# Kernel optimization log

Measured on AMD Instinct MI355X. Metric: run time of the kernel, lower is better.

Reference implementation:

```python
import jax, jax.numpy as jnp
import numpy as np

HIDDEN = 1024
MSG = 1024
T = 3
B = 256
N = 80  # num_categories


def setup_inputs() -> dict:
    key = jax.random.key(0)
    ks = jax.random.split(key, 10)
    s = 0.02
    return {
        "x": jax.random.normal(ks[0], (B, N), dtype=jnp.float32),
        # msg_update_fn: Linear(hidden->msg) + ReLU
        "W1": jax.random.normal(ks[1], (MSG, HIDDEN), dtype=jnp.float32) * s,
        "b1": jax.random.normal(ks[2], (MSG,), dtype=jnp.float32) * s,
        # GRUCell(msg_dim -> hidden_dim), torch layout [3*hidden, in]
        "Wih": jax.random.normal(ks[3], (3 * HIDDEN, MSG), dtype=jnp.float32) * s,
        "Whh": jax.random.normal(ks[4], (3 * HIDDEN, HIDDEN), dtype=jnp.float32) * s,
        "bih": jax.random.normal(ks[5], (3 * HIDDEN,), dtype=jnp.float32) * s,
        "bhh": jax.random.normal(ks[6], (3 * HIDDEN,), dtype=jnp.float32) * s,
        # Conv1d(hidden, 1, kernel=1) == per-position linear projection
        "w_s": jax.random.normal(ks[7], (HIDDEN,), dtype=jnp.float32) * s,
        "b_s": jax.random.normal(ks[8], (), dtype=jnp.float32) * s,
    }


def _gru_cell(msg, h, Wih, Whh, bih, bhh):
    # torch GRUCell: gate order (r, z, n)
    gi = msg @ Wih.T + bih  # [rows, 3H]
    gh = h @ Whh.T + bhh
    i_r, i_z, i_n = jnp.split(gi, 3, axis=-1)
    h_r, h_z, h_n = jnp.split(gh, 3, axis=-1)
    r = jax.nn.sigmoid(i_r + h_r)
    z = jax.nn.sigmoid(i_z + h_z)
    n = jnp.tanh(i_n + r * h_n)
    return (1.0 - z) * n + z * h


def reference(x, W1, b1, Wih, Whh, bih, bhh, w_s, b_s):
    batch, num_cat = x.shape
    pad_left = (HIDDEN - 1) // 2
    # hidden_0: each scalar label embedded at position pad_left of a zero vector
    hidden = jnp.zeros((batch, num_cat, HIDDEN), dtype=x.dtype).at[:, :, pad_left].set(x)
    for _ in range(T):
        m = jax.nn.relu(jnp.einsum("bnh,mh->bnm", hidden, W1) + b1)  # [B,N,MSG]
        # all-pairs masked mean over j != i  ==  (total sum - self) / (N-1)
        msg = (jnp.sum(m, axis=1, keepdims=True) - m) / (num_cat - 1)
        hidden = _gru_cell(
            msg.reshape(-1, MSG), hidden.reshape(-1, HIDDEN), Wih, Whh, bih, bhh
        ).reshape(batch, num_cat, HIDDEN)
    # Conv1d(hidden->1, k=1) over [B, hidden, N] then squeeze -> [B, N]
    return jnp.einsum("bnh,h->bn", hidden, w_s) + b_s
```

## Files before the change

kernel.cpp:

```cpp
#include <hip/hip_runtime.h>
#include <cstdint>
#include <cstddef>

#define HID 1024
#define NB 256
#define NCAT 80
#define ROWS (NB*NCAT)
#define PADL 511

typedef short short8_t __attribute__((ext_vector_type(8)));
typedef float f32x4_t __attribute__((ext_vector_type(4)));
typedef unsigned short u16;
typedef u16 u16x8_t __attribute__((ext_vector_type(8)));
typedef u16 u16x4_t __attribute__((ext_vector_type(4)));
typedef float f32x4v_t __attribute__((ext_vector_type(4)));

typedef const __attribute__((address_space(1))) unsigned int guint_t;
typedef __attribute__((address_space(3))) unsigned int luint_t;

__device__ __forceinline__ void gl_lds16(const void* g, void* l) {
  __builtin_amdgcn_global_load_lds((guint_t*)g, (luint_t*)l, 16, 0, 0);
}

__device__ __forceinline__ u16 f2bf(float f) {
  unsigned u = __float_as_uint(f);
  u += 0x7fffu + ((u >> 16) & 1u);
  return (u16)(u >> 16);
}
__device__ __forceinline__ float bf2f(u16 s) {
  return __uint_as_float(((unsigned)s) << 16);
}

__device__ __forceinline__ f32x4_t mfma16(short8_t a, short8_t b, f32x4_t c) {
  return __builtin_amdgcn_mfma_f32_16x16x32_bf16(a, b, c, 0, 0, 0);
}

__global__ void cvt_w_kernel(const float* __restrict__ W1, const float* __restrict__ Wih,
                             const float* __restrict__ Whh, u16* __restrict__ W1b,
                             u16* __restrict__ Wihb, u16* __restrict__ Whhb) {
  int idx = blockIdx.x * 256 + threadIdx.x;
  const float* src; u16* dst; int off;
  if (idx < 262144) { src = W1; dst = W1b; off = idx; }
  else if (idx < 1048576) { src = Wih; dst = Wihb; off = idx - 262144; }
  else { src = Whh; dst = Whhb; off = idx - 1048576; }
  f32x4v_t v = reinterpret_cast<const f32x4v_t*>(src)[off];
  u16 o0 = f2bf(v[0]), o1 = f2bf(v[1]), o2 = f2bf(v[2]), o3 = f2bf(v[3]);
  u16* d = dst + (size_t)off * 4;
  d[0] = o0; d[1] = o1; d[2] = o2; d[3] = o3;
}

__global__ void m1_kernel(const float* __restrict__ x, const float* __restrict__ W1,
                          const float* __restrict__ b1, u16* __restrict__ mb) {
  long idx = (long)blockIdx.x * 256 + threadIdx.x;
  long e = idx * 8;
  int r = (int)(e >> 10); int c0 = (int)(e & 1023);
  float xv = x[r];
  u16x8_t o;
#pragma unroll
  for (int j = 0; j < 8; j++) {
    int c = c0 + j;
    float v = xv * W1[(size_t)c * 1024 + PADL] + b1[c];
    o[j] = f2bf(v > 0.f ? v : 0.f);
  }
  *reinterpret_cast<u16x8_t*>(mb + e) = o;
}

__global__ void seg_msg_kernel(u16* __restrict__ mb) {
  int b = blockIdx.x;
  int c0 = blockIdx.y * 512 + threadIdx.x * 4;
  u16* base = mb + (size_t)b * (NCAT * 1024) + c0;
  float s0 = 0.f, s1 = 0.f, s2 = 0.f, s3 = 0.f;
#pragma unroll 4
  for (int n = 0; n < NCAT; n++) {
    u16x4_t v = *reinterpret_cast<const u16x4_t*>(base + (size_t)n * 1024);
    s0 += bf2f(v[0]); s1 += bf2f(v[1]); s2 += bf2f(v[2]); s3 += bf2f(v[3]);
  }
  const float inv = 1.0f / (NCAT - 1);
#pragma unroll 4
  for (int n = 0; n < NCAT; n++) {
    u16x4_t v = *reinterpret_cast<const u16x4_t*>(base + (size_t)n * 1024);
    u16x4_t o;
    o[0] = f2bf((s0 - bf2f(v[0])) * inv);
    o[1] = f2bf((s1 - bf2f(v[1])) * inv);
    o[2] = f2bf((s2 - bf2f(v[2])) * inv);
    o[3] = f2bf((s3 - bf2f(v[3])) * inv);
    *reinterpret_cast<u16x4_t*>(base + (size_t)n * 1024) = o;
  }
}

__device__ __forceinline__ void gm_stage(int kb, char* dstbase, const u16* hb,
                                         const u16* W1b, int rb, int nb, int tid) {
#pragma unroll
  for (int i = 0; i < 4; i++) {
    int c = tid + i * 256;
    const u16* src;
    if (c < 512) {
      int r = c >> 2, s = c & 3;
      int sp = s ^ ((r >> 1) & 3);
      src = hb + ((size_t)(rb * 128 + r)) * 1024 + kb * 32 + sp * 8;
    } else {
      int w = c - 512; int r = w >> 2, s = w & 3;
      int sp = s ^ ((r >> 1) & 3);
      src = W1b + ((size_t)(nb * 128 + r)) * 1024 + kb * 32 + sp * 8;
    }
    gl_lds16(src, dstbase + c * 16);
  }
}

__launch_bounds__(256, 4)
__global__ void gemm_m_kernel(const u16* __restrict__ hb, const u16* __restrict__ W1b,
                              const float* __restrict__ b1, u16* __restrict__ mb) {
  __shared__ __attribute__((aligned(128))) char lds[32768];
  const int tid = threadIdx.x;
  const int rb = blockIdx.x, nb = blockIdx.y;
  const int wid = tid >> 6, lane = tid & 63;
  const int wr = wid >> 1, wc = wid & 1;
  const int lr = lane & 15, ls = lane >> 4;
  const int swoff = (ls ^ ((lr >> 1) & 3)) * 16;
  f32x4_t acc[4][4];
  f32x4_t z4 = {0.f, 0.f, 0.f, 0.f};
#pragma unroll
  for (int m2 = 0; m2 < 4; m2++)
#pragma unroll
    for (int n2 = 0; n2 < 4; n2++) acc[m2][n2] = z4;

  gm_stage(0, lds, hb, W1b, rb, nb, tid);
  __syncthreads();
  int cur = 0;
  for (int kb = 0; kb < 32; kb++) {
    char* bc = lds + cur * 16384;
    if (kb + 1 < 32) gm_stage(kb + 1, lds + (cur ^ 1) * 16384, hb, W1b, rb, nb, tid);
    short8_t a[4], bw[4];
#pragma unroll
    for (int m2 = 0; m2 < 4; m2++) {
      int row = wr * 64 + m2 * 16 + lr;
      a[m2] = *reinterpret_cast<const short8_t*>(bc + row * 64 + swoff);
    }
#pragma unroll
    for (int n2 = 0; n2 < 4; n2++) {
      int r = wc * 64 + n2 * 16 + lr;
      bw[n2] = *reinterpret_cast<const short8_t*>(bc + 8192 + r * 64 + swoff);
    }
#pragma unroll
    for (int m2 = 0; m2 < 4; m2++)
#pragma unroll
      for (int n2 = 0; n2 < 4; n2++)
        acc[m2][n2] = mfma16(a[m2], bw[n2], acc[m2][n2]);
    __syncthreads();
    cur ^= 1;
  }
#pragma unroll
  for (int m2 = 0; m2 < 4; m2++)
#pragma unroll
    for (int n2 = 0; n2 < 4; n2++) {
      int col = nb * 128 + wc * 64 + n2 * 16 + lr;
      float bias = b1[col];
#pragma unroll
      for (int j = 0; j < 4; j++) {
        int gr = rb * 128 + wr * 64 + m2 * 16 + ls * 4 + j;
        float v = acc[m2][n2][j] + bias;
        mb[(size_t)gr * 1024 + col] = f2bf(v > 0.f ? v : 0.f);
      }
    }
}

template <int FIRST>
__device__ __forceinline__ void gru_stage(int kb, char* dstbase,
    const u16* msgb, const u16* hbin, const u16* Wihb, const u16* Whhb,
    int rb, int hb0, int tid) {
  const u16* Ap; const u16* Wp; int kk;
  if (FIRST) { Ap = msgb; Wp = Wihb; kk = kb; }
  else if (kb < 32) { Ap = msgb; Wp = Wihb; kk = kb; }
  else { Ap = hbin; Wp = Whhb; kk = kb - 32; }
#pragma unroll
  for (int i = 0; i < 3; i++) {
    int c = tid + i * 512;
    if (c < 1280) {
      const u16* src; char* dst;
      if (c < 512) {
        int r = c >> 2, s = c & 3;
        int sp = s ^ ((r >> 1) & 3);
        src = Ap + ((size_t)(rb * 128 + r)) * 1024 + kk * 32 + sp * 8;
        dst = dstbase + c * 16;
      } else {
        int w = c - 512;
        int g = w >> 8, r = (w >> 2) & 63, s = w & 3;
        int sp = s ^ ((r >> 1) & 3);
        src = Wp + ((size_t)(g * 1024 + hb0 + r)) * 1024 + kk * 32 + sp * 8;
        dst = dstbase + 8192 + w * 16;
      }
      gl_lds16(src, dst);
    }
  }
}

template <int FIRST>
__launch_bounds__(512, 4)
__global__ void gru_kernel(const u16* __restrict__ msgb, const u16* __restrict__ hbin,
                           const u16* __restrict__ Wihb, const u16* __restrict__ Whhb,
                           const float* __restrict__ bih, const float* __restrict__ bhh,
                           const float* __restrict__ x, const float* __restrict__ WhhF,
                           float* __restrict__ hf, u16* __restrict__ hbout) {
  __shared__ __attribute__((aligned(128))) char lds[40960];
  const int tid = threadIdx.x;
  const int rb = blockIdx.x;
  const int hb0 = blockIdx.y * 64;
  const int wid = tid >> 6, lane = tid & 63;
  const int wr = wid >> 1, wc = wid & 1;
  const int lr = lane & 15, ls = lane >> 4;
  const int swoff = (ls ^ ((lr >> 1) & 3)) * 16;

  f32x4_t ar[2][2], az[2][2], ain[2][2], ahn[2][2];
  f32x4_t z4 = {0.f, 0.f, 0.f, 0.f};
#pragma unroll
  for (int m2 = 0; m2 < 2; m2++)
#pragma unroll
    for (int n2 = 0; n2 < 2; n2++) { ar[m2][n2] = z4; az[m2][n2] = z4; ain[m2][n2] = z4; ahn[m2][n2] = z4; }

  const int NK = FIRST ? 32 : 64;
  gru_stage<FIRST>(0, lds, msgb, hbin, Wihb, Whhb, rb, hb0, tid);
  __syncthreads();
  int cur = 0;
  for (int kb = 0; kb < NK; kb++) {
    char* bc = lds + cur * 20480;
    if (kb + 1 < NK)
      gru_stage<FIRST>(kb + 1, lds + (cur ^ 1) * 20480, msgb, hbin, Wihb, Whhb, rb, hb0, tid);

    short8_t a[2], br_[2], bz_[2], bn_[2];
#pragma unroll
    for (int m2 = 0; m2 < 2; m2++) {
      int row = wr * 32 + m2 * 16 + lr;
      a[m2] = *reinterpret_cast<const short8_t*>(bc + row * 64 + swoff);
    }
#pragma unroll
    for (int n2 = 0; n2 < 2; n2++) {
      int r = wc * 32 + n2 * 16 + lr;
      br_[n2] = *reinterpret_cast<const short8_t*>(bc + 8192 + r * 64 + swoff);
      bz_[n2] = *reinterpret_cast<const short8_t*>(bc + 12288 + r * 64 + swoff);
      bn_[n2] = *reinterpret_cast<const short8_t*>(bc + 16384 + r * 64 + swoff);
    }
    const bool second = (!FIRST) && (kb >= 32);
#pragma unroll
    for (int m2 = 0; m2 < 2; m2++)
#pragma unroll
      for (int n2 = 0; n2 < 2; n2++) {
        ar[m2][n2] = mfma16(a[m2], br_[n2], ar[m2][n2]);
        az[m2][n2] = mfma16(a[m2], bz_[n2], az[m2][n2]);
        if (second) ahn[m2][n2] = mfma16(a[m2], bn_[n2], ahn[m2][n2]);
        else        ain[m2][n2] = mfma16(a[m2], bn_[n2], ain[m2][n2]);
      }
    __syncthreads();
    cur ^= 1;
  }

#pragma unroll
  for (int n2 = 0; n2 < 2; n2++) {
    int ch = hb0 + wc * 32 + n2 * 16 + lr;
    float br_ = bih[ch] + bhh[ch];
    float bz_ = bih[1024 + ch] + bhh[1024 + ch];
    float bin_ = bih[2048 + ch];
    float bhn_ = bhh[2048 + ch];
    float wr511 = 0.f, wz511 = 0.f, wn511 = 0.f;
    if (FIRST) {
      wr511 = WhhF[(size_t)ch * 1024 + PADL];
      wz511 = WhhF[(size_t)(1024 + ch) * 1024 + PADL];
      wn511 = WhhF[(size_t)(2048 + ch) * 1024 + PADL];
    }
#pragma unroll
    for (int m2 = 0; m2 < 2; m2++)
#pragma unroll
      for (int j = 0; j < 4; j++) {
        int gr = rb * 128 + wr * 32 + m2 * 16 + ls * 4 + j;
        float vr = ar[m2][n2][j] + br_;
        float vz = az[m2][n2][j] + bz_;
        float vin = ain[m2][n2][j] + bin_;
        float vhn, hold;
        if (FIRST) {
          float xv = x[gr];
          vr += xv * wr511;
          vz += xv * wz511;
          vhn = xv * wn511 + bhn_;
          hold = (ch == PADL) ? xv : 0.f;
        } else {
          vhn = ahn[m2][n2][j] + bhn_;
          hold = hf[(size_t)gr * 1024 + ch];
        }
        float rg = 1.f / (1.f + __expf(-vr));
        float zg = 1.f / (1.f + __expf(-vz));
        float ng = tanhf(vin + rg * vhn);
        float hnew = (1.f - zg) * ng + zg * hold;
        hf[(size_t)gr * 1024 + ch] = hnew;
        hbout[(size_t)gr * 1024 + ch] = f2bf(hnew);
      }
  }
}

__global__ void out_proj_kernel(const float* __restrict__ hf, const float* __restrict__ wsv,
                                const float* __restrict__ bs, float* __restrict__ out) {
  int row = blockIdx.x * 4 + (threadIdx.x >> 6);
  int lane = threadIdx.x & 63;
  const float* p = hf + (size_t)row * 1024;
  float s = 0.f;
#pragma unroll
  for (int t = 0; t < 16; t++) s += p[lane + t * 64] * wsv[lane + t * 64];
#pragma unroll
  for (int off = 32; off; off >>= 1) s += __shfl_down(s, off);
  if (lane == 0) out[row] = s + bs[0];
}

extern "C" void kernel_launch(void* const* d_in, const int* in_sizes, int n_in,
                              void* d_out, int out_size, void* d_ws, size_t ws_size,
                              hipStream_t stream) {
  const float* x = (const float*)d_in[0];
  const float* W1 = (const float*)d_in[1];
  const float* b1 = (const float*)d_in[2];
  const float* Wih = (const float*)d_in[3];
  const float* Whh = (const float*)d_in[4];
  const float* bih = (const float*)d_in[5];
  const float* bhh = (const float*)d_in[6];
  const float* wsv = (const float*)d_in[7];
  const float* bs = (const float*)d_in[8];
  float* out = (float*)d_out;

  char* wsp = (char*)d_ws;
  size_t off = 0;
  auto alloc = [&](size_t bytes) { void* p = wsp + off; off += (bytes + 255) & ~(size_t)255; return p; };
  float* hf = (float*)alloc((size_t)ROWS * 1024 * 4);
  u16* hbA = (u16*)alloc((size_t)ROWS * 1024 * 2);
  u16* hbB = (u16*)alloc((size_t)ROWS * 1024 * 2);
  u16* mb = (u16*)alloc((size_t)ROWS * 1024 * 2);
  u16* W1b = (u16*)alloc((size_t)1024 * 1024 * 2);
  u16* Wihb = (u16*)alloc((size_t)3072 * 1024 * 2);
  u16* Whhb = (u16*)alloc((size_t)3072 * 1024 * 2);

  cvt_w_kernel<<<7168, 256, 0, stream>>>(W1, Wih, Whh, W1b, Wihb, Whhb);

  m1_kernel<<<10240, 256, 0, stream>>>(x, W1, b1, mb);
  seg_msg_kernel<<<dim3(NB, 2), 128, 0, stream>>>(mb);
  gru_kernel<1><<<dim3(160, 16), 512, 0, stream>>>(mb, nullptr, Wihb, Whhb, bih, bhh, x, Whh, hf, hbA);

  for (int it = 1; it < 3; it++) {
    u16* hin = (it & 1) ? hbA : hbB;
    u16* hout = (it & 1) ? hbB : hbA;
    gemm_m_kernel<<<dim3(160, 8), 256, 0, stream>>>(hin, W1b, b1, mb);
    seg_msg_kernel<<<dim3(NB, 2), 128, 0, stream>>>(mb);
    gru_kernel<0><<<dim3(160, 16), 512, 0, stream>>>(mb, hin, Wihb, Whhb, bih, bhh, x, Whh, hf, hout);
  }

  out_proj_kernel<<<5120, 256, 0, stream>>>(hf, wsv, bs, out);
}
```

Measured before the change: 1.037 ms.

## Enlarge GRU GEMM tile to 256 rows with unrolled double-buffered pipeline

New measurement: 981.4 us. 5.4% less time.

```diff
diff --git a/kernel.cpp b/kernel.cpp
--- a/kernel.cpp
+++ b/kernel.cpp
@@ -164,125 +164,131 @@
     }
 }
 
-template <int FIRST>
-__device__ __forceinline__ void gru_stage(int kb, char* dstbase,
-    const u16* msgb, const u16* hbin, const u16* Wihb, const u16* Whhb,
-    int rb, int hb0, int tid) {
-  const u16* Ap; const u16* Wp; int kk;
-  if (FIRST) { Ap = msgb; Wp = Wihb; kk = kb; }
-  else if (kb < 32) { Ap = msgb; Wp = Wihb; kk = kb; }
-  else { Ap = hbin; Wp = Whhb; kk = kb - 32; }
-#pragma unroll
-  for (int i = 0; i < 3; i++) {
-    int c = tid + i * 512;
-    if (c < 1280) {
-      const u16* src; char* dst;
-      if (c < 512) {
-        int r = c >> 2, s = c & 3;
-        int sp = s ^ ((r >> 1) & 3);
-        src = Ap + ((size_t)(rb * 128 + r)) * 1024 + kk * 32 + sp * 8;
-        dst = dstbase + c * 16;
-      } else {
-        int w = c - 512;
-        int g = w >> 8, r = (w >> 2) & 63, s = w & 3;
-        int sp = s ^ ((r >> 1) & 3);
-        src = Wp + ((size_t)(g * 1024 + hb0 + r)) * 1024 + kk * 32 + sp * 8;
-        dst = dstbase + 8192 + w * 16;
-      }
-      gl_lds16(src, dst);
-    }
-  }
-}
-
-template <int FIRST>
-__launch_bounds__(512, 4)
+template <int NSEG>
+__launch_bounds__(512, 2)
 __global__ void gru_kernel(const u16* __restrict__ msgb, const u16* __restrict__ hbin,
                            const u16* __restrict__ Wihb, const u16* __restrict__ Whhb,
                            const float* __restrict__ bih, const float* __restrict__ bhh,
                            const float* __restrict__ x, const float* __restrict__ WhhF,
                            float* __restrict__ hf, u16* __restrict__ hbout) {
-  __shared__ __attribute__((aligned(128))) char lds[40960];
+  __shared__ __attribute__((aligned(128))) char lds[57344];
   const int tid = threadIdx.x;
   const int rb = blockIdx.x;
   const int hb0 = blockIdx.y * 64;
   const int wid = tid >> 6, lane = tid & 63;
-  const int wr = wid >> 1, wc = wid & 1;
+  const int mw = wid >> 1, nw = wid & 1;
   const int lr = lane & 15, ls = lane >> 4;
   const int swoff = (ls ^ ((lr >> 1) & 3)) * 16;
 
-  f32x4_t ar[2][2], az[2][2], ain[2][2], ahn[2][2];
+  const int slot = tid & 3;
+  const int r0 = tid >> 2;
+  const int sp16 = (slot ^ ((r0 >> 1) & 3)) * 16;
+  const char* sA0 = (const char*)msgb + ((size_t)(rb * 256 + r0) << 11) + sp16;
+  const char* sA1 = (const char*)msgb + ((size_t)(rb * 256 + 128 + r0) << 11) + sp16;
+  const int g2 = r0 >> 6, c2 = r0 & 63;
+  const char* sW2 = (const char*)Wihb + ((size_t)(g2 * 1024 + hb0 + c2) << 11) + sp16;
+  const char* sW3 = (const char*)Wihb + ((size_t)(2048 + hb0 + (r0 & 63)) << 11) + sp16;
+  const int d0 = tid * 16, d1 = d0 + 8192, d2 = d0 + 16384, d3 = d0 + 24576;
+
+#define STAGE(BUF) do { \
+    gl_lds16(sA0, (BUF) + d0); gl_lds16(sA1, (BUF) + d1); gl_lds16(sW2, (BUF) + d2); \
+    if (tid < 256) gl_lds16(sW3, (BUF) + d3); \
+    sA0 += 64; sA1 += 64; sW2 += 64; sW3 += 64; } while (0)
+
+  int offA[4], offB[3][2];
+#pragma unroll
+  for (int m = 0; m < 4; m++) offA[m] = (mw * 64 + m * 16 + lr) * 64 + swoff;
+#pragma unroll
+  for (int g = 0; g < 3; g++)
+#pragma unroll
+    for (int n = 0; n < 2; n++)
+      offB[g][n] = 16384 + (g * 64 + nw * 32 + n * 16 + lr) * 64 + swoff;
+
+  f32x4_t ar[4][2], az[4][2], an0[4][2], an1[4][2];
   f32x4_t z4 = {0.f, 0.f, 0.f, 0.f};
 #pragma unroll
-  for (int m2 = 0; m2 < 2; m2++)
-#pragma unroll
-    for (int n2 = 0; n2 < 2; n2++) { ar[m2][n2] = z4; az[m2][n2] = z4; ain[m2][n2] = z4; ahn[m2][n2] = z4; }
-
-  const int NK = FIRST ? 32 : 64;
-  gru_stage<FIRST>(0, lds, msgb, hbin, Wihb, Whhb, rb, hb0, tid);
+  for (int m = 0; m < 4; m++)
+#pragma unroll
+    for (int n = 0; n < 2; n++) { ar[m][n] = z4; az[m][n] = z4; an0[m][n] = z4; an1[m][n] = z4; }
+
+#define COMPUTE(BUF, AN) do { \
+    short8_t a_[4], bR_[2], bZ_[2], bN_[2]; \
+    _Pragma("unroll") for (int m = 0; m < 4; m++) \
+      a_[m] = *reinterpret_cast<const short8_t*>((BUF) + offA[m]); \
+    _Pragma("unroll") for (int n = 0; n < 2; n++) { \
+      bR_[n] = *reinterpret_cast<const short8_t*>((BUF) + offB[0][n]); \
+      bZ_[n] = *reinterpret_cast<const short8_t*>((BUF) + offB[1][n]); \
+      bN_[n] = *reinterpret_cast<const short8_t*>((BUF) + offB[2][n]); } \
+    _Pragma("unroll") for (int m = 0; m < 4; m++) \
+    _Pragma("unroll") for (int n = 0; n < 2; n++) { \
+      ar[m][n] = mfma16(a_[m], bR_[n], ar[m][n]); \
+      az[m][n] = mfma16(a_[m], bZ_[n], az[m][n]); \
+      AN[m][n] = mfma16(a_[m], bN_[n], AN[m][n]); } \
+  } while (0)
+
+  char* bufA = lds;
+  char* bufB = lds + 28672;
+
+  STAGE(bufA);
   __syncthreads();
-  int cur = 0;
-  for (int kb = 0; kb < NK; kb++) {
-    char* bc = lds + cur * 20480;
-    if (kb + 1 < NK)
-      gru_stage<FIRST>(kb + 1, lds + (cur ^ 1) * 20480, msgb, hbin, Wihb, Whhb, rb, hb0, tid);
-
-    short8_t a[2], br_[2], bz_[2], bn_[2];
-#pragma unroll
-    for (int m2 = 0; m2 < 2; m2++) {
-      int row = wr * 32 + m2 * 16 + lr;
-      a[m2] = *reinterpret_cast<const short8_t*>(bc + row * 64 + swoff);
-    }
-#pragma unroll
-    for (int n2 = 0; n2 < 2; n2++) {
-      int r = wc * 32 + n2 * 16 + lr;
-      br_[n2] = *reinterpret_cast<const short8_t*>(bc + 8192 + r * 64 + swoff);
-      bz_[n2] = *reinterpret_cast<const short8_t*>(bc + 12288 + r * 64 + swoff);
-      bn_[n2] = *reinterpret_cast<const short8_t*>(bc + 16384 + r * 64 + swoff);
-    }
-    const bool second = (!FIRST) && (kb >= 32);
-#pragma unroll
-    for (int m2 = 0; m2 < 2; m2++)
-#pragma unroll
-      for (int n2 = 0; n2 < 2; n2++) {
-        ar[m2][n2] = mfma16(a[m2], br_[n2], ar[m2][n2]);
-        az[m2][n2] = mfma16(a[m2], bz_[n2], az[m2][n2]);
-        if (second) ahn[m2][n2] = mfma16(a[m2], bn_[n2], ahn[m2][n2]);
-        else        ain[m2][n2] = mfma16(a[m2], bn_[n2], ain[m2][n2]);
-      }
+  for (int kb = 0; kb < 32; kb += 2) {
+    STAGE(bufB);
+    COMPUTE(bufA, an0);
     __syncthreads();
-    cur ^= 1;
-  }
+    if (kb != 30) {
+      STAGE(bufA);
+    } else if (NSEG == 2) {
+      const ptrdiff_t dA = (const char*)hbin - (const char*)msgb - 2048;
+      const ptrdiff_t dW = (const char*)Whhb - (const char*)Wihb - 2048;
+      sA0 += dA; sA1 += dA; sW2 += dW; sW3 += dW;
+      STAGE(bufA);
+    }
+    COMPUTE(bufB, an0);
+    __syncthreads();
+  }
+  if (NSEG == 2) {
+    for (int kb = 0; kb < 32; kb += 2) {
+      STAGE(bufB);
+      COMPUTE(bufA, an1);
+      __syncthreads();
+      if (kb != 30) STAGE(bufA);
+      COMPUTE(bufB, an1);
+      __syncthreads();
+    }
+  }
+#undef STAGE
+#undef COMPUTE
 
 #pragma unroll
   for (int n2 = 0; n2 < 2; n2++) {
-    int ch = hb0 + wc * 32 + n2 * 16 + lr;
+    int ch = hb0 + nw * 32 + n2 * 16 + lr;
     float br_ = bih[ch] + bhh[ch];
     float bz_ = bih[1024 + ch] + bhh[1024 + ch];
     float bin_ = bih[2048 + ch];
     float bhn_ = bhh[2048 + ch];
     float wr511 = 0.f, wz511 = 0.f, wn511 = 0.f;
-    if (FIRST) {
+    if (NSEG == 1) {
       wr511 = WhhF[(size_t)ch * 1024 + PADL];
       wz511 = WhhF[(size_t)(1024 + ch) * 1024 + PADL];
       wn511 = WhhF[(size_t)(2048 + ch) * 1024 + PADL];
     }
 #pragma unroll
-    for (int m2 = 0; m2 < 2; m2++)
+    for (int m = 0; m < 4; m++)
 #pragma unroll
       for (int j = 0; j < 4; j++) {
-        int gr = rb * 128 + wr * 32 + m2 * 16 + ls * 4 + j;
-        float vr = ar[m2][n2][j] + br_;
-        float vz = az[m2][n2][j] + bz_;
-        float vin = ain[m2][n2][j] + bin_;
+        int gr = rb * 256 + mw * 64 + m * 16 + ls * 4 + j;
+        float vr = ar[m][n2][j] + br_;
+        float vz = az[m][n2][j] + bz_;
+        float vin = an0[m][n2][j] + bin_;
         float vhn, hold;
-        if (FIRST) {
+        if (NSEG == 1) {
           float xv = x[gr];
           vr += xv * wr511;
           vz += xv * wz511;
           vhn = xv * wn511 + bhn_;
           hold = (ch == PADL) ? xv : 0.f;
         } else {
-          vhn = ahn[m2][n2][j] + bhn_;
+          vhn = an1[m][n2][j] + bhn_;
           hold = hf[(size_t)gr * 1024 + ch];
         }
         float rg = 1.f / (1.f + __expf(-vr));
@@ -337,14 +343,14 @@
 
   m1_kernel<<<10240, 256, 0, stream>>>(x, W1, b1, mb);
   seg_msg_kernel<<<dim3(NB, 2), 128, 0, stream>>>(mb);
-  gru_kernel<1><<<dim3(160, 16), 512, 0, stream>>>(mb, nullptr, Wihb, Whhb, bih, bhh, x, Whh, hf, hbA);
+  gru_kernel<1><<<dim3(80, 16), 512, 0, stream>>>(mb, nullptr, Wihb, Whhb, bih, bhh, x, Whh, hf, hbA);
 
   for (int it = 1; it < 3; it++) {
     u16* hin = (it & 1) ? hbA : hbB;
     u16* hout = (it & 1) ? hbB : hbA;
     gemm_m_kernel<<<dim3(160, 8), 256, 0, stream>>>(hin, W1b, b1, mb);
     seg_msg_kernel<<<dim3(NB, 2), 128, 0, stream>>>(mb);
-    gru_kernel<0><<<dim3(160, 16), 512, 0, stream>>>(mb, hin, Wihb, Whhb, bih, bhh, x, Whh, hf, hout);
+    gru_kernel<0 + 2><<<dim3(80, 16), 512, 0, stream>>>(mb, hin, Wihb, Whhb, bih, bhh, x, Whh, hf, hout);
   }
 
   out_proj_kernel<<<5120, 256, 0, stream>>>(hf, wsv, bs, out);
```
